# Kernel tuning notes

Hardware: AMD Instinct MI355X
Metric: run time of the kernel (lower is better)

Reference implementation:

```python
import jax, jax.numpy as jnp
import numpy as np

B, T, N_EMBD = 4, 2048, 1024
N_EXP, TOP_K = 8, 2
EPS = 1e-9
EVAL_CAPACITY_FACTOR = 2.0
MIN_CAPACITY = 4
# eval-mode capacity: min(group_size, int(group_size * cap_factor / n_exp)), floored at min_capacity
CAPACITY = max(min(T, int(T * EVAL_CAPACITY_FACTOR / N_EXP)), MIN_CAPACITY)  # 512
THRESHOLD = np.array([EPS, 0.2], dtype=np.float32)  # threshold_eval buffer: [eps, *thresholds]


def setup_inputs() -> dict:
    key = jax.random.key(0)
    k1, k2, k3 = jax.random.split(key, 3)
    x = jax.random.normal(k1, (B, T, N_EMBD), dtype=jnp.float32)
    w_g = jax.random.normal(k2, (N_EXP, N_EMBD), dtype=jnp.float32) * 0.02
    probs = jax.random.uniform(k3, (TOP_K, B, T), dtype=jnp.float32)
    return {"x": x, "w_g": w_g, "probs": probs}


def reference(x, w_g, probs):
    # gate logits and softmax gates
    gate_logits = jnp.einsum('btd,ed->bte', x, w_g)          # [B,T,E]
    raw_gates = jax.nn.softmax(gate_logits, axis=-1)
    top_v, top_i = jax.lax.top_k(raw_gates, TOP_K)           # [B,T,k]
    gates = jnp.transpose(top_v, (2, 0, 1))                  # [k,B,T]
    gate_idx = jnp.transpose(top_i, (2, 0, 1))               # [k,B,T]
    one_hot_gate = jax.nn.one_hot(gate_idx, N_EXP, dtype=jnp.float32)  # [k,B,T,E]

    # renormalize top-k gates
    denom = jnp.clip(jnp.sum(gates, axis=0, keepdims=True), EPS, None)
    gates = gates / denom

    # stochastic thresholding (top-1 always routes)
    thr = jnp.asarray(THRESHOLD)[:, None, None]              # [k,1,1]
    should_route = probs < gates / jnp.clip(thr, EPS, None)
    should_route = should_route.at[0].set(True)
    mask = one_hot_gate * should_route[..., None].astype(jnp.float32)  # [k,B,T,E]

    # exclusive cumsum over tokens (dim T)
    mask_cumsum = jnp.cumsum(mask, axis=-2) - mask           # [k,B,T,E]

    masks, positions = [], []
    prev = jnp.zeros((B, 1, N_EXP), dtype=jnp.float32)
    cap_f = float(CAPACITY)
    for n in range(TOP_K):  # small fixed loop over routing ranks
        pos = (mask_cumsum[n] + prev) * mask[n]              # [B,T,E]
        m_n = mask[n] * (pos < cap_f).astype(jnp.float32)    # capacity drop
        prev = jnp.sum(m_n, axis=1, keepdims=True) + prev
        masks.append(m_n)
        positions.append(jnp.sum(pos, axis=-1))              # [B,T]
    mask = jnp.stack(masks)                                  # [k,B,T,E]
    positions = jnp.stack(positions)                         # [k,B,T]

    mask_flat = jnp.sum(mask, axis=-1)                       # [k,B,T] in {0,1}
    gates = gates * mask_flat

    # position one-hot; out-of-range positions map to all-zero rows (== safe_one_hot + slice)
    pos_oh = jax.nn.one_hot(positions.astype(jnp.int32), CAPACITY, dtype=jnp.float32)  # [k,B,T,C]

    # combine tensor: sum over k of gates * mask_flat * one_hot(expert) x one_hot(position)
    combine = jnp.einsum('kbt,kbte,kbtc->btec', gates * mask_flat, one_hot_gate, pos_oh)  # [B,T,E,C]

    dispatch_hard = (combine > 0).astype(combine.dtype)
    # straight-through dispatch tensor
    dispatch = dispatch_hard + combine - jax.lax.stop_gradient(combine)
    return dispatch, combine
```

## Files before the change

### kernel.cpp

```cpp
#include <hip/hip_runtime.h>

#define BB 4
#define TT 2048
#define DD 1024
#define EE 8
#define CAP 512
#define NTOK (BB*TT)
#define OUT_HALF ((size_t)NTOK * EE * CAP)

__global__ __launch_bounds__(256) void gate_kernel(
    const float* __restrict__ x, const float* __restrict__ w,
    const float* __restrict__ probs,
    int* __restrict__ e0, int* __restrict__ e1, int* __restrict__ r1,
    float* __restrict__ v0, float* __restrict__ v1)
{
    const int wave = threadIdx.x >> 6;
    const int lane = threadIdx.x & 63;
    const int token = blockIdx.x * 4 + wave;
    const float* xt = x + (size_t)token * DD;

    float acc[EE];
    #pragma unroll
    for (int e = 0; e < EE; ++e) acc[e] = 0.f;

    #pragma unroll 4
    for (int i = 0; i < DD / 64; ++i) {
        float xv = xt[i * 64 + lane];
        #pragma unroll
        for (int e = 0; e < EE; ++e)
            acc[e] = fmaf(xv, w[e * DD + i * 64 + lane], acc[e]);
    }
    #pragma unroll
    for (int e = 0; e < EE; ++e) {
        #pragma unroll
        for (int off = 32; off > 0; off >>= 1)
            acc[e] += __shfl_xor(acc[e], off, 64);
    }

    if (lane == 0) {
        float mx = acc[0];
        #pragma unroll
        for (int e = 1; e < EE; ++e) mx = fmaxf(mx, acc[e]);
        float ex[EE]; float Z = 0.f;
        #pragma unroll
        for (int e = 0; e < EE; ++e) { ex[e] = expf(acc[e] - mx); Z += ex[e]; }
        int i0 = 0;
        #pragma unroll
        for (int e = 1; e < EE; ++e) if (ex[e] > ex[i0]) i0 = e;
        int i1 = (i0 == 0) ? 1 : 0;
        #pragma unroll
        for (int e = 0; e < EE; ++e) if (e != i0 && ex[e] > ex[i1]) i1 = e;
        float t0 = ex[i0] / Z, t1 = ex[i1] / Z;
        float den = fmaxf(t0 + t1, 1e-9f);
        float g0 = t0 / den, g1 = t1 / den;
        float p1 = probs[NTOK + token];
        int route = (p1 < g1 / 0.2f) ? 1 : 0;
        e0[token] = i0; e1[token] = i1; r1[token] = route;
        v0[token] = g0; v1[token] = g1;
    }
}

__global__ __launch_bounds__(1024) void scan_kernel(
    int* __restrict__ e0, int* __restrict__ e1, const int* __restrict__ r1,
    const float* __restrict__ v0, const float* __restrict__ v1)
{
    const int b = blockIdx.x;
    const int tid = threadIdx.x;
    const int wave = tid >> 6;
    const int lane = tid & 63;

    __shared__ int cnt[16][EE];
    __shared__ int off[16][EE];
    __shared__ int base[EE];

    if (tid < EE) base[tid] = 0;
    __syncthreads();

    for (int k = 0; k < 2; ++k) {
        for (int chunk = 0; chunk < 2; ++chunk) {
            const int t = chunk * 1024 + tid;
            const int gidx = b * TT + t;
            int e; bool active;
            if (k == 0) { e = e0[gidx]; active = true; }
            else        { e = e1[gidx]; active = (r1[gidx] != 0); }

            if (tid < 16 * EE) cnt[tid >> 3][tid & 7] = 0;
            __syncthreads();

            unsigned long long act = __ballot(active);
            unsigned long long m = act;
            #pragma unroll
            for (int bit = 0; bit < 3; ++bit) {
                unsigned long long bm = __ballot((e >> bit) & 1);
                m &= ((e >> bit) & 1) ? bm : ~bm;
            }
            int rank = __popcll(m & ((1ull << lane) - 1ull));
            if (active && rank == 0) cnt[wave][e] = __popcll(m);
            __syncthreads();

            if (tid < EE) {
                int run = base[tid];
                #pragma unroll
                for (int w = 0; w < 16; ++w) { off[w][tid] = run; run += cnt[w][tid]; }
                base[tid] = run;
            }
            __syncthreads();

            int tgt = -1;
            if (active) {
                int pos = off[wave][e] + rank;
                if (pos < CAP) tgt = e * CAP + pos;
            }
            if (k == 0) e0[gidx] = tgt; else e1[gidx] = tgt;
            __syncthreads();
        }
        if (k == 0) {
            if (tid < EE) base[tid] = min(base[tid], CAP);
            __syncthreads();
        }
    }
}

__global__ __launch_bounds__(256) void fill_scatter_kernel(
    const int* __restrict__ t0, const int* __restrict__ t1,
    const float* __restrict__ v0, const float* __restrict__ v1,
    float4* __restrict__ out)
{
    const int token = blockIdx.x;
    const int tid = threadIdx.x;
    const int a0 = t0[token];
    const int a1 = t1[token];
    const float g0 = v0[token];
    const float g1 = v1[token];

    float4* drow = out + (size_t)token * 1024;
    float4* crow = out + (OUT_HALF / 4) + (size_t)token * 1024;

    #pragma unroll
    for (int i = 0; i < 4; ++i) {
        const int f = i * 1024 + tid * 4;
        float4 d, c;
        d.x = (f + 0 == a0 || f + 0 == a1) ? 1.f : 0.f;
        d.y = (f + 1 == a0 || f + 1 == a1) ? 1.f : 0.f;
        d.z = (f + 2 == a0 || f + 2 == a1) ? 1.f : 0.f;
        d.w = (f + 3 == a0 || f + 3 == a1) ? 1.f : 0.f;
        c.x = (f + 0 == a0) ? g0 : ((f + 0 == a1) ? g1 : 0.f);
        c.y = (f + 1 == a0) ? g0 : ((f + 1 == a1) ? g1 : 0.f);
        c.z = (f + 2 == a0) ? g0 : ((f + 2 == a1) ? g1 : 0.f);
        c.w = (f + 3 == a0) ? g0 : ((f + 3 == a1) ? g1 : 0.f);
        drow[i * 256 + tid] = d;
        crow[i * 256 + tid] = c;
    }
}

extern "C" void kernel_launch(void* const* d_in, const int* in_sizes, int n_in,
                              void* d_out, int out_size, void* d_ws, size_t ws_size,
                              hipStream_t stream) {
    const float* x     = (const float*)d_in[0];
    const float* w     = (const float*)d_in[1];
    const float* probs = (const float*)d_in[2];
    float* out = (float*)d_out;

    int*   e0 = (int*)d_ws;
    int*   e1 = e0 + NTOK;
    int*   r1 = e1 + NTOK;
    float* v0 = (float*)(r1 + NTOK);
    float* v1 = v0 + NTOK;

    gate_kernel<<<2048, 256, 0, stream>>>(x, w, probs, e0, e1, r1, v0, v1);
    scan_kernel<<<4, 1024, 0, stream>>>(e0, e1, r1, v0, v1);
    fill_scatter_kernel<<<8192, 256, 0, stream>>>(e0, e1, v0, v1, (float4*)out);
}
```

Measured before the change: 68.19 us.

## Parallelize capacity scan per (batch, expert) wave and vectorize gate loads

The scan kernel is restructured from 4 blocks of 1024 threads with shared-memory prefix sums and many barriers into 32 single-wave blocks, one per (batch, expert) pair. Each wave counts its expert's tokens with ballot and popcount, and writes targets to separate buffers. The routing flag is packed into the second expert index. The gate kernel also switches to float4 loads for x and w. This removes barrier-heavy serial work on very few CUs, but the whole run is likely dominated by the 256MB output fill.

```diff
diff --git a/kernel.cpp b/kernel.cpp
--- a/kernel.cpp
+++ b/kernel.cpp
@@ -11,24 +11,30 @@
 __global__ __launch_bounds__(256) void gate_kernel(
     const float* __restrict__ x, const float* __restrict__ w,
     const float* __restrict__ probs,
-    int* __restrict__ e0, int* __restrict__ e1, int* __restrict__ r1,
+    int* __restrict__ e0, int* __restrict__ e1enc,
     float* __restrict__ v0, float* __restrict__ v1)
 {
     const int wave = threadIdx.x >> 6;
     const int lane = threadIdx.x & 63;
     const int token = blockIdx.x * 4 + wave;
-    const float* xt = x + (size_t)token * DD;
+    const float4* xt4 = (const float4*)(x + (size_t)token * DD);
+    const float4* w4  = (const float4*)w;
 
     float acc[EE];
     #pragma unroll
     for (int e = 0; e < EE; ++e) acc[e] = 0.f;
 
-    #pragma unroll 4
-    for (int i = 0; i < DD / 64; ++i) {
-        float xv = xt[i * 64 + lane];
+    #pragma unroll
+    for (int i = 0; i < 4; ++i) {
+        float4 xv = xt4[i * 64 + lane];
         #pragma unroll
-        for (int e = 0; e < EE; ++e)
-            acc[e] = fmaf(xv, w[e * DD + i * 64 + lane], acc[e]);
+        for (int e = 0; e < EE; ++e) {
+            float4 wv = w4[e * 256 + i * 64 + lane];
+            acc[e] = fmaf(xv.x, wv.x, acc[e]);
+            acc[e] = fmaf(xv.y, wv.y, acc[e]);
+            acc[e] = fmaf(xv.z, wv.z, acc[e]);
+            acc[e] = fmaf(xv.w, wv.w, acc[e]);
+        }
     }
     #pragma unroll
     for (int e = 0; e < EE; ++e) {
@@ -55,69 +61,54 @@
         float g0 = t0 / den, g1 = t1 / den;
         float p1 = probs[NTOK + token];
         int route = (p1 < g1 / 0.2f) ? 1 : 0;
-        e0[token] = i0; e1[token] = i1; r1[token] = route;
+        e0[token] = i0;
+        e1enc[token] = i1 | (route << 3);
         v0[token] = g0; v1[token] = g1;
     }
 }
 
-__global__ __launch_bounds__(1024) void scan_kernel(
-    int* __restrict__ e0, int* __restrict__ e1, const int* __restrict__ r1,
-    const float* __restrict__ v0, const float* __restrict__ v1)
+__global__ __launch_bounds__(64) void scan_kernel(
+    const int* __restrict__ e0, const int* __restrict__ e1enc,
+    int* __restrict__ t0, int* __restrict__ t1)
 {
-    const int b = blockIdx.x;
-    const int tid = threadIdx.x;
-    const int wave = tid >> 6;
-    const int lane = tid & 63;
+    const int b = blockIdx.x >> 3;
+    const int e = blockIdx.x & 7;
+    const int lane = threadIdx.x;
+    const unsigned long long lt = (lane == 63) ? 0x7fffffffffffffffull
+                                               : ((1ull << lane) - 1ull);
+    const int base_tok = b * TT;
 
-    __shared__ int cnt[16][EE];
-    __shared__ int off[16][EE];
-    __shared__ int base[EE];
+    int ev[32];
+    #pragma unroll
+    for (int c = 0; c < 32; ++c) ev[c] = e0[base_tok + c * 64 + lane];
 
-    if (tid < EE) base[tid] = 0;
-    __syncthreads();
+    int cnt = 0;
+    #pragma unroll
+    for (int c = 0; c < 32; ++c) {
+        bool hit = (ev[c] == e);
+        unsigned long long m = __ballot(hit);
+        if (hit) {
+            int pos = cnt + __popcll(m & lt);
+            t0[base_tok + c * 64 + lane] = (pos < CAP) ? e * CAP + pos : -1;
+        }
+        cnt += __popcll(m);
+    }
 
-    for (int k = 0; k < 2; ++k) {
-        for (int chunk = 0; chunk < 2; ++chunk) {
-            const int t = chunk * 1024 + tid;
-            const int gidx = b * TT + t;
-            int e; bool active;
-            if (k == 0) { e = e0[gidx]; active = true; }
-            else        { e = e1[gidx]; active = (r1[gidx] != 0); }
+    int e1v[32];
+    #pragma unroll
+    for (int c = 0; c < 32; ++c) e1v[c] = e1enc[base_tok + c * 64 + lane];
 
-            if (tid < 16 * EE) cnt[tid >> 3][tid & 7] = 0;
-            __syncthreads();
-
-            unsigned long long act = __ballot(active);
-            unsigned long long m = act;
-            #pragma unroll
-            for (int bit = 0; bit < 3; ++bit) {
-                unsigned long long bm = __ballot((e >> bit) & 1);
-                m &= ((e >> bit) & 1) ? bm : ~bm;
-            }
-            int rank = __popcll(m & ((1ull << lane) - 1ull));
-            if (active && rank == 0) cnt[wave][e] = __popcll(m);
-            __syncthreads();
-
-            if (tid < EE) {
-                int run = base[tid];
-                #pragma unroll
-                for (int w = 0; w < 16; ++w) { off[w][tid] = run; run += cnt[w][tid]; }
-                base[tid] = run;
-            }
-            __syncthreads();
-
-            int tgt = -1;
-            if (active) {
-                int pos = off[wave][e] + rank;
-                if (pos < CAP) tgt = e * CAP + pos;
-            }
-            if (k == 0) e0[gidx] = tgt; else e1[gidx] = tgt;
-            __syncthreads();
+    int cnt1 = min(cnt, CAP);
+    #pragma unroll
+    for (int c = 0; c < 32; ++c) {
+        bool sel = ((e1v[c] & 7) == e);
+        bool hit = sel && (e1v[c] & 8);
+        unsigned long long m = __ballot(hit);
+        if (sel) {
+            int pos = cnt1 + __popcll(m & lt);
+            t1[base_tok + c * 64 + lane] = (hit && pos < CAP) ? e * CAP + pos : -1;
         }
-        if (k == 0) {
-            if (tid < EE) base[tid] = min(base[tid], CAP);
-            __syncthreads();
-        }
+        cnt1 += __popcll(m);
     }
 }
 
@@ -163,11 +154,12 @@
 
     int*   e0 = (int*)d_ws;
     int*   e1 = e0 + NTOK;
-    int*   r1 = e1 + NTOK;
-    float* v0 = (float*)(r1 + NTOK);
+    int*   t0 = e1 + NTOK;
+    int*   t1 = t0 + NTOK;
+    float* v0 = (float*)(t1 + NTOK);
     float* v1 = v0 + NTOK;
 
-    gate_kernel<<<2048, 256, 0, stream>>>(x, w, probs, e0, e1, r1, v0, v1);
-    scan_kernel<<<4, 1024, 0, stream>>>(e0, e1, r1, v0, v1);
-    fill_scatter_kernel<<<8192, 256, 0, stream>>>(e0, e1, v0, v1, (float4*)out);
+    gate_kernel<<<2048, 256, 0, stream>>>(x, w, probs, e0, e1, v0, v1);
+    scan_kernel<<<32, 64, 0, stream>>>(e0, e1, t0, t1);
+    fill_scatter_kernel<<<8192, 256, 0, stream>>>(t0, t1, v0, v1, (float4*)out);
 }
```

Result: no change. 68.41 us (+0.3%).
